# Performance work log

Hardware: AMD Instinct MI355X
Metric: run time of the kernel (lower is better)

## Reference

```python
import jax, jax.numpy as jnp
import numpy as np

DN = ('NCHW', 'OIHW', 'NCHW')

def _conv(x, w, groups=1, padding=0):
    return jax.lax.conv_general_dilated(
        x, w, window_strides=(1, 1), padding=[(padding, padding)] * 2,
        dimension_numbers=DN, feature_group_count=groups)

def _bn(x, scale, shift):
    # precomputed inference BN: x * scale + shift, per channel (NCHW)
    return x * scale[None, :, None, None] + shift[None, :, None, None]

def _channel_shuffle(x, g):
    n, c, h, w = x.shape
    return x.reshape(n, g, c // g, h, w).transpose(0, 2, 1, 3, 4).reshape(n, c, h, w)

def setup_inputs() -> dict:
    key = jax.random.key(0)
    ks = jax.random.split(key, 13)
    N, Cin, H, W = 32, 240, 56, 56
    Cout, G = 480, 3
    mid = Cout // 4  # 120
    inp = {
        'x': jax.random.normal(ks[0], (N, Cin, H, W), jnp.float32),
        'w1': jax.random.normal(ks[1], (mid, Cin // G, 1, 1), jnp.float32) * 0.05,
        'scale1': jax.random.uniform(ks[2], (mid,), jnp.float32, 0.5, 1.5),
        'shift1': jax.random.normal(ks[3], (mid,), jnp.float32) * 0.1,
        'w2': jax.random.normal(ks[4], (mid, 1, 3, 3), jnp.float32) * 0.05,
        'scale2': jax.random.uniform(ks[5], (mid,), jnp.float32, 0.5, 1.5),
        'shift2': jax.random.normal(ks[6], (mid,), jnp.float32) * 0.1,
        'w3': jax.random.normal(ks[7], (Cout, mid // G, 1, 1), jnp.float32) * 0.05,
        'scale3': jax.random.uniform(ks[8], (Cout,), jnp.float32, 0.5, 1.5),
        'shift3': jax.random.normal(ks[9], (Cout,), jnp.float32) * 0.1,
        'wsc': jax.random.normal(ks[10], (Cout, Cin, 1, 1), jnp.float32) * 0.05,
        'scale_sc': jax.random.uniform(ks[11], (Cout,), jnp.float32, 0.5, 1.5),
        'shift_sc': jax.random.normal(ks[12], (Cout,), jnp.float32) * 0.1,
        'groups': G,
    }
    return inp

def reference(x, w1, scale1, shift1, w2, scale2, shift2, w3, scale3, shift3,
              wsc, scale_sc, shift_sc, groups):
    g = int(groups)
    mid = w1.shape[0]
    # conv1 (grouped 1x1) -> fused BN + ReLU
    y = _conv(x, w1, groups=g)
    y = jax.nn.relu(_bn(y, scale1, shift1))
    # conv2 (depthwise 3x3) -> fused BN + channel shuffle
    y = _conv(y, w2, groups=mid, padding=1)
    y = _channel_shuffle(_bn(y, scale2, shift2), g)
    # conv3 (grouped 1x1)
    y = _conv(y, w3, groups=g)
    # shortcut: 1x1 conv (in_channels != out_channels)
    z = _conv(x, wsc)
    # fused final: relu(BN3(y)) + BN_sc(z)
    return jax.nn.relu(_bn(y, scale3, shift3)) + _bn(z, scale_sc, shift_sc)
```

## Files before the change

kernel.cpp:

```cpp
#include <hip/hip_runtime.h>

typedef short bf16x8 __attribute__((ext_vector_type(8)));
typedef float f32x4 __attribute__((ext_vector_type(4)));

namespace {
constexpr int kN = 32;
constexpr int kCin = 240;
constexpr int kHW = 3136;
constexpr int kMid = 120;
constexpr int kCout = 480;
constexpr size_t kXbtBytes = (size_t)kN * kHW * 240 * 2;
constexpr size_t kY2Off = kXbtBytes;
constexpr size_t kY2Bytes = (size_t)kN * kHW * 120 * 2;
constexpr size_t kY1Off = kY2Off + kY2Bytes;
}

__device__ __align__(16) unsigned short g_w1b[3 * 48 * 96];
__device__ __align__(16) unsigned short g_wscb[480 * 256];
__device__ __align__(16) unsigned short g_w3b[480 * 64];

static __device__ __forceinline__ unsigned short f2b(float f) {
  unsigned u = __float_as_uint(f);
  u = (u + 0x7fffu + ((u >> 16) & 1u)) >> 16;
  return (unsigned short)u;
}
static __device__ __forceinline__ float b2f(unsigned short s) {
  return __uint_as_float(((unsigned)s) << 16);
}
static __device__ __forceinline__ f32x4 mfma16(bf16x8 a, bf16x8 b, f32x4 c) {
  return __builtin_amdgcn_mfma_f32_16x16x32_bf16(a, b, c, 0, 0, 0);
}

__global__ __launch_bounds__(256) void prep_weights(
    const float* __restrict__ w1, const float* __restrict__ wsc,
    const float* __restrict__ w3) {
  const int idx = blockIdx.x * 256 + threadIdx.x;
  if (idx < 3 * 48 * 96) {
    const int g = idx / (48 * 96), r = idx % (48 * 96), j = r / 96, c = r % 96;
    g_w1b[idx] =
        (j < 40 && c < 80) ? f2b(w1[(g * 40 + j) * 80 + c]) : (unsigned short)0;
  } else if (idx < 3 * 48 * 96 + 480 * 256) {
    const int i = idx - 3 * 48 * 96;
    const int co = i >> 8, c = i & 255;
    g_wscb[i] = (c < 240) ? f2b(wsc[co * 240 + c]) : (unsigned short)0;
  } else if (idx < 3 * 48 * 96 + 480 * 256 + 480 * 64) {
    const int i = idx - (3 * 48 * 96 + 480 * 256);
    const int co = i >> 6, s = i & 63;
    g_w3b[i] = (s < 40) ? f2b(w3[co * 40 + s]) : (unsigned short)0;
  }
}

__global__ __launch_bounds__(256) void transpose_cast_x(
    const float* __restrict__ x, unsigned short* __restrict__ xbt) {
  const int pt = blockIdx.x % 13;
  const int ct = (blockIdx.x / 13) % 15;
  const int n = blockIdx.x / (13 * 15);
  const int p = pt * 256 + threadIdx.x;
  if (p >= kHW) return;
  const float* xp = x + ((size_t)n * kCin + ct * 16) * kHW + p;
  unsigned short v[16];
#pragma unroll
  for (int r = 0; r < 16; ++r) v[r] = f2b(xp[(size_t)r * kHW]);
  unsigned short* dst = xbt + (size_t)(n * kHW + p) * 240 + ct * 16;
  *reinterpret_cast<int4*>(dst) = *reinterpret_cast<const int4*>(v);
  *reinterpret_cast<int4*>(dst + 8) = *reinterpret_cast<const int4*>(v + 8);
}

__global__ __launch_bounds__(256) void conv1_gemm(
    const unsigned short* __restrict__ xbt, const float* __restrict__ scale1,
    const float* __restrict__ shift1, unsigned short* __restrict__ y1b) {
  const int pt = blockIdx.x % 49;
  const int g = (blockIdx.x / 49) % 3;
  const int n = blockIdx.x / (49 * 3);
  const int P0 = pt * 64;
  const int lane = threadIdx.x & 63;
  const int wv = threadIdx.x >> 6;
  const int l15 = lane & 15, quad = lane >> 4;

  f32x4 acc[3];
#pragma unroll
  for (int nt = 0; nt < 3; ++nt) acc[nt] = (f32x4){0.f, 0.f, 0.f, 0.f};

  const unsigned short* abase =
      xbt + (size_t)(n * kHW + P0 + wv * 16 + l15) * 240 + g * 80 + quad * 8;
  const unsigned short* bbase = g_w1b + (g * 48 + l15) * 96 + quad * 8;
#pragma unroll
  for (int ks = 0; ks < 3; ++ks) {
    const bf16x8 a = *reinterpret_cast<const bf16x8*>(abase + ks * 32);
#pragma unroll
    for (int nt = 0; nt < 3; ++nt) {
      const bf16x8 b =
          *reinterpret_cast<const bf16x8*>(bbase + nt * 16 * 96 + ks * 32);
      acc[nt] = mfma16(a, b, acc[nt]);
    }
  }

  __shared__ unsigned short lds[48 * 72];
#pragma unroll
  for (int nt = 0; nt < 3; ++nt) {
    const int j = nt * 16 + l15;
    if (j < 40) {
      const int c = g * 40 + j;
      const float sc = scale1[c], sh = shift1[c];
#pragma unroll
      for (int r = 0; r < 4; ++r) {
        float v = fmaf(acc[nt][r], sc, sh);
        v = v > 0.f ? v : 0.f;
        lds[j * 72 + wv * 16 + quad * 4 + r] = f2b(v);
      }
    }
  }
  __syncthreads();
  unsigned short* yb = y1b + ((size_t)n * kMid + g * 40) * kHW;
#pragma unroll
  for (int i = 0; i < 10; ++i) {
    const int e = threadIdx.x + i * 256;
    const int c = e >> 6, pp = e & 63;
    yb[(size_t)c * kHW + P0 + pp] = lds[c * 72 + pp];
  }
}

__global__ __launch_bounds__(256) void dw_bn_shuffle(
    const unsigned short* __restrict__ y1b, const float* __restrict__ w2,
    const float* __restrict__ scale2, const float* __restrict__ shift2,
    unsigned short* __restrict__ y2t) {
  const int h = blockIdx.x % 56;
  const int n = blockIdx.x / 56;
  __shared__ unsigned short lds[120 * 58];
  const unsigned short* yb = y1b + (size_t)n * kMid * kHW;
  for (int idx = threadIdx.x; idx < 120 * 56; idx += 256) {
    const int c = idx / 56, w = idx % 56;
    float acc = 0.f;
    const unsigned short* ip = yb + (size_t)c * kHW;
    const float* wp = w2 + c * 9;
#pragma unroll
    for (int dy = 0; dy < 3; ++dy) {
      const int hh = h + dy - 1;
      if (hh < 0 || hh >= 56) continue;
#pragma unroll
      for (int dx = 0; dx < 3; ++dx) {
        const int ww = w + dx - 1;
        if (ww < 0 || ww >= 56) continue;
        acc = fmaf(b2f(ip[hh * 56 + ww]), wp[dy * 3 + dx], acc);
      }
    }
    const float v = fmaf(acc, scale2[c], shift2[c]);
    const int cn = (c % 40) * 3 + c / 40;
    lds[cn * 58 + w] = f2b(v);
  }
  __syncthreads();
  unsigned short* dst = y2t + (size_t)(n * kHW + h * 56) * 120;
  for (int e = threadIdx.x; e < 56 * 120; e += 256)
    dst[e] = lds[(e % 120) * 58 + (e / 120)];
}

__global__ __launch_bounds__(256) void conv3_sc_gemm(
    const unsigned short* __restrict__ xbt,
    const unsigned short* __restrict__ y2t, const float* __restrict__ scale3,
    const float* __restrict__ shift3, const float* __restrict__ ssc,
    const float* __restrict__ bsc, float* __restrict__ out) {
  const int pt = blockIdx.x % 49;
  const int cb = (blockIdx.x / 49) % 3;
  const int n = blockIdx.x / (49 * 3);
  const int P0 = pt * 64;
  const int lane = threadIdx.x & 63;
  const int wv = threadIdx.x >> 6;
  const int mh = wv & 1, nh = wv >> 1;
  const int l15 = lane & 15, quad = lane >> 4;

  f32x4 acc_sc[2][5], acc_c3[2][5];
#pragma unroll
  for (int ms = 0; ms < 2; ++ms)
#pragma unroll
    for (int nt = 0; nt < 5; ++nt) {
      acc_sc[ms][nt] = (f32x4){0.f, 0.f, 0.f, 0.f};
      acc_c3[ms][nt] = (f32x4){0.f, 0.f, 0.f, 0.f};
    }

  const int co_row = cb * 160 + nh * 80 + l15;
  {
    const size_t prow = (size_t)(n * kHW + P0 + mh * 32 + l15) * 240;
    const unsigned short* a0 = xbt + prow + quad * 8;
    const unsigned short* a1 = xbt + prow + 16 * 240 + quad * 8;
    const unsigned short* b0 = g_wscb + co_row * 256 + quad * 8;
#pragma unroll
    for (int ks = 0; ks < 8; ++ks) {
      const bf16x8 A0 = *reinterpret_cast<const bf16x8*>(a0 + ks * 32);
      const bf16x8 A1 = *reinterpret_cast<const bf16x8*>(a1 + ks * 32);
#pragma unroll
      for (int nt = 0; nt < 5; ++nt) {
        const bf16x8 B =
            *reinterpret_cast<const bf16x8*>(b0 + nt * 16 * 256 + ks * 32);
        acc_sc[0][nt] = mfma16(A0, B, acc_sc[0][nt]);
        acc_sc[1][nt] = mfma16(A1, B, acc_sc[1][nt]);
      }
    }
  }
  {
    const size_t qrow = (size_t)(n * kHW + P0 + mh * 32 + l15) * 120 + cb * 40;
    const unsigned short* a0 = y2t + qrow + quad * 8;
    const unsigned short* a1 = y2t + qrow + 16 * 120 + quad * 8;
    const unsigned short* b3 = g_w3b + co_row * 64 + quad * 8;
#pragma unroll
    for (int ks = 0; ks < 2; ++ks) {
      const bf16x8 A0 = *reinterpret_cast<const bf16x8*>(a0 + ks * 32);
      const bf16x8 A1 = *reinterpret_cast<const bf16x8*>(a1 + ks * 32);
#pragma unroll
      for (int nt = 0; nt < 5; ++nt) {
        const bf16x8 B =
            *reinterpret_cast<const bf16x8*>(b3 + nt * 16 * 64 + ks * 32);
        acc_c3[0][nt] = mfma16(A0, B, acc_c3[0][nt]);
        acc_c3[1][nt] = mfma16(A1, B, acc_c3[1][nt]);
      }
    }
  }
  float* ob = out + (size_t)n * kCout * kHW;
#pragma unroll
  for (int nt = 0; nt < 5; ++nt) {
    const int co = cb * 160 + nh * 80 + nt * 16 + l15;
    const float s3 = scale3[co], h3 = shift3[co];
    const float s_ = ssc[co], h_ = bsc[co];
#pragma unroll
    for (int ms = 0; ms < 2; ++ms) {
      float4 r;
      float* op = ob + (size_t)co * kHW + P0 + mh * 32 + ms * 16 + quad * 4;
      float* rp = reinterpret_cast<float*>(&r);
#pragma unroll
      for (int r4 = 0; r4 < 4; ++r4) {
        float v3 = fmaf(acc_c3[ms][nt][r4], s3, h3);
        v3 = v3 > 0.f ? v3 : 0.f;
        rp[r4] = v3 + fmaf(acc_sc[ms][nt][r4], s_, h_);
      }
      *reinterpret_cast<float4*>(op) = r;
    }
  }
}

extern "C" void kernel_launch(void* const* d_in, const int* in_sizes, int n_in,
                              void* d_out, int out_size, void* d_ws,
                              size_t ws_size, hipStream_t stream) {
  const float* x = (const float*)d_in[0];
  const float* w1 = (const float*)d_in[1];
  const float* scale1 = (const float*)d_in[2];
  const float* shift1 = (const float*)d_in[3];
  const float* w2 = (const float*)d_in[4];
  const float* scale2 = (const float*)d_in[5];
  const float* shift2 = (const float*)d_in[6];
  const float* w3 = (const float*)d_in[7];
  const float* scale3 = (const float*)d_in[8];
  const float* shift3 = (const float*)d_in[9];
  const float* wsc = (const float*)d_in[10];
  const float* ssc = (const float*)d_in[11];
  const float* bsc = (const float*)d_in[12];
  float* out = (float*)d_out;

  unsigned short* xbt = (unsigned short*)d_ws;
  unsigned short* y2t = (unsigned short*)((char*)d_ws + kY2Off);
  unsigned short* y1b = (unsigned short*)((char*)d_ws + kY1Off);

  prep_weights<<<654, 256, 0, stream>>>(w1, wsc, w3);
  transpose_cast_x<<<32 * 15 * 13, 256, 0, stream>>>(x, xbt);
  conv1_gemm<<<32 * 3 * 49, 256, 0, stream>>>(xbt, scale1, shift1, y1b);
  dw_bn_shuffle<<<32 * 56, 256, 0, stream>>>(y1b, w2, scale2, shift2, y2t);
  conv3_sc_gemm<<<32 * 3 * 49, 256, 0, stream>>>(xbt, y2t, scale3, shift3, ssc,
                                                 bsc, out);
}
```

Baseline: 533.1 us.

## Fuse conv1 into depthwise kernel, tile-interleave activations, merge conv3/shortcut accumulators

Rewrites the pipeline. Activations are stored in an MFMA-friendly interleaved 16-pixel tile layout. The grouped 1x1 conv1 is fused into the depthwise 3x3 kernel, which recomputes conv1 for the needed rows into LDS instead of writing and re-reading a y1 buffer. The final GEMM folds the conv3 BN/ReLU result into a single accumulator by pre-dividing by the shortcut scale and uses larger pixel tiles across batch boundaries. This removes one intermediate round trip through global memory and halves accumulator registers, at the cost of redundant conv1 work on halo rows, larger LDS use, and a division by scale_sc that fails if that scale is zero.

Result: faster. 479.7 us (-10.0%).

```diff
diff --git a/kernel.cpp b/kernel.cpp
--- a/kernel.cpp
+++ b/kernel.cpp
@@ -4,135 +4,150 @@
 typedef float f32x4 __attribute__((ext_vector_type(4)));
 
 namespace {
-constexpr int kN = 32;
-constexpr int kCin = 240;
 constexpr int kHW = 3136;
-constexpr int kMid = 120;
-constexpr int kCout = 480;
-constexpr size_t kXbtBytes = (size_t)kN * kHW * 240 * 2;
-constexpr size_t kY2Off = kXbtBytes;
-constexpr size_t kY2Bytes = (size_t)kN * kHW * 120 * 2;
-constexpr size_t kY1Off = kY2Off + kY2Bytes;
-}
-
-__device__ __align__(16) unsigned short g_w1b[3 * 48 * 96];
-__device__ __align__(16) unsigned short g_wscb[480 * 256];
-__device__ __align__(16) unsigned short g_w3b[480 * 64];
+constexpr int kNPx = 32 * kHW;
+constexpr int kPtiles = kNPx / 16;
+constexpr size_t kXbiShorts = (size_t)kPtiles * 4096;
+}
+
+__device__ __align__(16) unsigned short g_w1i[3 * 4 * 48 * 32];
+__device__ __align__(16) unsigned short g_wsci[8 * 480 * 32];
+__device__ __align__(16) unsigned short g_w3i[2 * 480 * 32];
 
 static __device__ __forceinline__ unsigned short f2b(float f) {
   unsigned u = __float_as_uint(f);
   u = (u + 0x7fffu + ((u >> 16) & 1u)) >> 16;
   return (unsigned short)u;
 }
-static __device__ __forceinline__ float b2f(unsigned short s) {
-  return __uint_as_float(((unsigned)s) << 16);
-}
 static __device__ __forceinline__ f32x4 mfma16(bf16x8 a, bf16x8 b, f32x4 c) {
   return __builtin_amdgcn_mfma_f32_16x16x32_bf16(a, b, c, 0, 0, 0);
+}
+static __device__ __forceinline__ bf16x8 ldg8(const unsigned short* p) {
+  return *reinterpret_cast<const bf16x8*>(p);
 }
 
 __global__ __launch_bounds__(256) void prep_weights(
     const float* __restrict__ w1, const float* __restrict__ wsc,
     const float* __restrict__ w3) {
   const int idx = blockIdx.x * 256 + threadIdx.x;
-  if (idx < 3 * 48 * 96) {
-    const int g = idx / (48 * 96), r = idx % (48 * 96), j = r / 96, c = r % 96;
-    g_w1b[idx] =
-        (j < 40 && c < 80) ? f2b(w1[(g * 40 + j) * 80 + c]) : (unsigned short)0;
-  } else if (idx < 3 * 48 * 96 + 480 * 256) {
-    const int i = idx - 3 * 48 * 96;
-    const int co = i >> 8, c = i & 255;
-    g_wscb[i] = (c < 240) ? f2b(wsc[co * 240 + c]) : (unsigned short)0;
-  } else if (idx < 3 * 48 * 96 + 480 * 256 + 480 * 64) {
-    const int i = idx - (3 * 48 * 96 + 480 * 256);
-    const int co = i >> 6, s = i & 63;
-    g_w3b[i] = (s < 40) ? f2b(w3[co * 40 + s]) : (unsigned short)0;
-  }
-}
-
-__global__ __launch_bounds__(256) void transpose_cast_x(
-    const float* __restrict__ x, unsigned short* __restrict__ xbt) {
-  const int pt = blockIdx.x % 13;
-  const int ct = (blockIdx.x / 13) % 15;
-  const int n = blockIdx.x / (13 * 15);
-  const int p = pt * 256 + threadIdx.x;
-  if (p >= kHW) return;
-  const float* xp = x + ((size_t)n * kCin + ct * 16) * kHW + p;
-  unsigned short v[16];
-#pragma unroll
-  for (int r = 0; r < 16; ++r) v[r] = f2b(xp[(size_t)r * kHW]);
-  unsigned short* dst = xbt + (size_t)(n * kHW + p) * 240 + ct * 16;
-  *reinterpret_cast<int4*>(dst) = *reinterpret_cast<const int4*>(v);
-  *reinterpret_cast<int4*>(dst + 8) = *reinterpret_cast<const int4*>(v + 8);
-}
-
-__global__ __launch_bounds__(256) void conv1_gemm(
-    const unsigned short* __restrict__ xbt, const float* __restrict__ scale1,
-    const float* __restrict__ shift1, unsigned short* __restrict__ y1b) {
-  const int pt = blockIdx.x % 49;
-  const int g = (blockIdx.x / 49) % 3;
-  const int n = blockIdx.x / (49 * 3);
-  const int P0 = pt * 64;
+  if (idx < 18432) {
+    const int g = idx / 6144, r = idx % 6144, kb = r / 1536;
+    const int j = (r % 1536) / 32, k = r % 32;
+    const int gk = g * 64 + kb * 32 + k;
+    const int c = gk - g * 80;
+    unsigned short v = 0;
+    if (j < 40 && c >= 0 && c < 80) v = f2b(w1[(g * 40 + j) * 80 + c]);
+    g_w1i[idx] = v;
+  } else if (idx < 18432 + 122880) {
+    const int i = idx - 18432;
+    const int kb = i / 15360, co = (i % 15360) / 32, k = i % 32;
+    const int c = kb * 32 + k;
+    g_wsci[i] = (c < 240) ? f2b(wsc[co * 240 + c]) : (unsigned short)0;
+  } else if (idx < 18432 + 122880 + 30720) {
+    const int i = idx - 141312;
+    const int kb = i / 15360, co = (i % 15360) / 32, k = i % 32;
+    const int cb = co / 160;
+    const int s = cb * 32 + kb * 32 + k - cb * 40;
+    g_w3i[i] = (s >= 0 && s < 40) ? f2b(w3[co * 40 + s]) : (unsigned short)0;
+  }
+}
+
+__global__ __launch_bounds__(256) void transpose_interleave(
+    const float* __restrict__ x, unsigned short* __restrict__ xbi) {
+  const int P0 = blockIdx.x * 64;
+  const int px_loc = threadIdx.x >> 2, part = threadIdx.x & 3;
+  const int P = P0 + px_loc;
+  const int n = P / kHW, hw = P % kHW;
+  const int pt = px_loc >> 4, l = px_loc & 15;
+  unsigned short* dst =
+      xbi + ((size_t)(P0 / 16) + pt) * 4096 + l * 32 + part * 8;
+  const float* xp = x + ((size_t)n * 240) * kHW + hw;
+#pragma unroll
+  for (int kb = 0; kb < 8; ++kb) {
+    unsigned short v[8];
+#pragma unroll
+    for (int j = 0; j < 8; ++j) {
+      const int c = kb * 32 + part * 8 + j;
+      v[j] = (c < 240) ? f2b(xp[(size_t)c * kHW]) : (unsigned short)0;
+    }
+    *reinterpret_cast<uint4*>(dst + kb * 512) =
+        *reinterpret_cast<const uint4*>(v);
+  }
+}
+
+__global__ __launch_bounds__(256) void conv1_dw_fused(
+    const unsigned short* __restrict__ xbi, const float* __restrict__ scale1,
+    const float* __restrict__ shift1, const float* __restrict__ w2,
+    const float* __restrict__ scale2, const float* __restrict__ shift2,
+    unsigned short* __restrict__ y2i) {
+  const int h = blockIdx.x % 56;
+  const int n = blockIdx.x / 56;
+  const int A0 = (h > 0) ? (((h - 1) * 56) & ~15) : 0;
+
+  __shared__ unsigned short lds_y1[192 * 120];
+  __shared__ float lds_w2[9 * 120];
+  __shared__ float lds_s2[120], lds_h2[120];
+
+  for (int i = threadIdx.x; i < 9 * 120; i += 256) {
+    const int tap = i / 120, c = i % 120;
+    lds_w2[i] = w2[c * 9 + tap];
+  }
+  if (threadIdx.x < 120) {
+    lds_s2[threadIdx.x] = scale2[threadIdx.x];
+    lds_h2[threadIdx.x] = shift2[threadIdx.x];
+  }
+
   const int lane = threadIdx.x & 63;
   const int wv = threadIdx.x >> 6;
   const int l15 = lane & 15, quad = lane >> 4;
-
-  f32x4 acc[3];
-#pragma unroll
-  for (int nt = 0; nt < 3; ++nt) acc[nt] = (f32x4){0.f, 0.f, 0.f, 0.f};
-
-  const unsigned short* abase =
-      xbt + (size_t)(n * kHW + P0 + wv * 16 + l15) * 240 + g * 80 + quad * 8;
-  const unsigned short* bbase = g_w1b + (g * 48 + l15) * 96 + quad * 8;
-#pragma unroll
-  for (int ks = 0; ks < 3; ++ks) {
-    const bf16x8 a = *reinterpret_cast<const bf16x8*>(abase + ks * 32);
+  const size_t PT = (size_t)(n * kHW + A0) / 16 + wv * 3;
+
+#pragma unroll
+  for (int g = 0; g < 3; ++g) {
+    f32x4 acc[3][3];
+#pragma unroll
+    for (int mt = 0; mt < 3; ++mt)
+#pragma unroll
+      for (int nt = 0; nt < 3; ++nt) acc[mt][nt] = (f32x4){0.f, 0.f, 0.f, 0.f};
+#pragma unroll
+    for (int kb = 0; kb < 4; ++kb) {
+      const int kbi = 2 * g + kb;
+      bf16x8 A[3];
+#pragma unroll
+      for (int mt = 0; mt < 3; ++mt)
+        A[mt] = ldg8(xbi + (PT + mt) * 4096 + kbi * 512 + l15 * 32 + quad * 8);
+#pragma unroll
+      for (int nt = 0; nt < 3; ++nt) {
+        const bf16x8 B = ldg8(g_w1i + (((g * 4 + kb) * 48) + nt * 16 + l15) * 32 +
+                              quad * 8);
+#pragma unroll
+        for (int mt = 0; mt < 3; ++mt) acc[mt][nt] = mfma16(A[mt], B, acc[mt][nt]);
+      }
+    }
 #pragma unroll
     for (int nt = 0; nt < 3; ++nt) {
-      const bf16x8 b =
-          *reinterpret_cast<const bf16x8*>(bbase + nt * 16 * 96 + ks * 32);
-      acc[nt] = mfma16(a, b, acc[nt]);
-    }
-  }
-
-  __shared__ unsigned short lds[48 * 72];
-#pragma unroll
-  for (int nt = 0; nt < 3; ++nt) {
-    const int j = nt * 16 + l15;
-    if (j < 40) {
-      const int c = g * 40 + j;
-      const float sc = scale1[c], sh = shift1[c];
-#pragma unroll
-      for (int r = 0; r < 4; ++r) {
-        float v = fmaf(acc[nt][r], sc, sh);
-        v = v > 0.f ? v : 0.f;
-        lds[j * 72 + wv * 16 + quad * 4 + r] = f2b(v);
+      const int j = nt * 16 + l15;
+      if (j < 40) {
+        const int c = g * 40 + j;
+        const float sc = scale1[c], sh = shift1[c];
+#pragma unroll
+        for (int mt = 0; mt < 3; ++mt) {
+          const int pxb = wv * 48 + mt * 16 + quad * 4;
+#pragma unroll
+          for (int r = 0; r < 4; ++r) {
+            float v = fmaf(acc[mt][nt][r], sc, sh);
+            v = v > 0.f ? v : 0.f;
+            lds_y1[(pxb + r) * 120 + c] = f2b(v);
+          }
+        }
       }
     }
   }
   __syncthreads();
-  unsigned short* yb = y1b + ((size_t)n * kMid + g * 40) * kHW;
-#pragma unroll
-  for (int i = 0; i < 10; ++i) {
-    const int e = threadIdx.x + i * 256;
-    const int c = e >> 6, pp = e & 63;
-    yb[(size_t)c * kHW + P0 + pp] = lds[c * 72 + pp];
-  }
-}
-
-__global__ __launch_bounds__(256) void dw_bn_shuffle(
-    const unsigned short* __restrict__ y1b, const float* __restrict__ w2,
-    const float* __restrict__ scale2, const float* __restrict__ shift2,
-    unsigned short* __restrict__ y2t) {
-  const int h = blockIdx.x % 56;
-  const int n = blockIdx.x / 56;
-  __shared__ unsigned short lds[120 * 58];
-  const unsigned short* yb = y1b + (size_t)n * kMid * kHW;
-  for (int idx = threadIdx.x; idx < 120 * 56; idx += 256) {
-    const int c = idx / 56, w = idx % 56;
-    float acc = 0.f;
-    const unsigned short* ip = yb + (size_t)c * kHW;
-    const float* wp = w2 + c * 9;
+
+  for (int idx = threadIdx.x; idx < 56 * 120; idx += 256) {
+    const int c = idx % 120, w = idx / 120;
+    float a = 0.f;
 #pragma unroll
     for (int dy = 0; dy < 3; ++dy) {
       const int hh = h + dy - 1;
@@ -141,97 +156,100 @@
       for (int dx = 0; dx < 3; ++dx) {
         const int ww = w + dx - 1;
         if (ww < 0 || ww >= 56) continue;
-        acc = fmaf(b2f(ip[hh * 56 + ww]), wp[dy * 3 + dx], acc);
-      }
-    }
-    const float v = fmaf(acc, scale2[c], shift2[c]);
+        const int pl = hh * 56 + ww - A0;
+        a = fmaf(__uint_as_float((unsigned)lds_y1[pl * 120 + c] << 16),
+                 lds_w2[(dy * 3 + dx) * 120 + c], a);
+      }
+    }
+    const float v = fmaf(a, lds_s2[c], lds_h2[c]);
     const int cn = (c % 40) * 3 + c / 40;
-    lds[cn * 58 + w] = f2b(v);
-  }
-  __syncthreads();
-  unsigned short* dst = y2t + (size_t)(n * kHW + h * 56) * 120;
-  for (int e = threadIdx.x; e < 56 * 120; e += 256)
-    dst[e] = lds[(e % 120) * 58 + (e / 120)];
-}
-
-__global__ __launch_bounds__(256) void conv3_sc_gemm(
-    const unsigned short* __restrict__ xbt,
-    const unsigned short* __restrict__ y2t, const float* __restrict__ scale3,
+    const int P = n * kHW + h * 56 + w;
+    y2i[((size_t)(P >> 4)) * 2048 + (cn >> 5) * 512 + (P & 15) * 32 +
+        (cn & 31)] = f2b(v);
+  }
+}
+
+__global__ __launch_bounds__(256, 3) void conv3_sc_gemm(
+    const unsigned short* __restrict__ xbi,
+    const unsigned short* __restrict__ y2i, const float* __restrict__ scale3,
     const float* __restrict__ shift3, const float* __restrict__ ssc,
     const float* __restrict__ bsc, float* __restrict__ out) {
-  const int pt = blockIdx.x % 49;
-  const int cb = (blockIdx.x / 49) % 3;
-  const int n = blockIdx.x / (49 * 3);
-  const int P0 = pt * 64;
+  const int pxb = blockIdx.x % 784;
+  const int cb = blockIdx.x / 784;
+  const int P0 = pxb * 128;
   const int lane = threadIdx.x & 63;
   const int wv = threadIdx.x >> 6;
   const int mh = wv & 1, nh = wv >> 1;
   const int l15 = lane & 15, quad = lane >> 4;
-
-  f32x4 acc_sc[2][5], acc_c3[2][5];
-#pragma unroll
-  for (int ms = 0; ms < 2; ++ms)
+  const int cbase = cb * 160 + nh * 80;
+
+  f32x4 acc[4][5];
+#pragma unroll
+  for (int mt = 0; mt < 4; ++mt)
+#pragma unroll
+    for (int nt = 0; nt < 5; ++nt) acc[mt][nt] = (f32x4){0.f, 0.f, 0.f, 0.f};
+
+  const size_t PT = (size_t)(P0 / 16) + mh * 4;
+
+#pragma unroll
+  for (int kb = 0; kb < 2; ++kb) {
+    const int kbi = cb + kb;
+    bf16x8 A[4];
+#pragma unroll
+    for (int mt = 0; mt < 4; ++mt)
+      A[mt] = ldg8(y2i + (PT + mt) * 2048 + kbi * 512 + l15 * 32 + quad * 8);
 #pragma unroll
     for (int nt = 0; nt < 5; ++nt) {
-      acc_sc[ms][nt] = (f32x4){0.f, 0.f, 0.f, 0.f};
-      acc_c3[ms][nt] = (f32x4){0.f, 0.f, 0.f, 0.f};
-    }
-
-  const int co_row = cb * 160 + nh * 80 + l15;
-  {
-    const size_t prow = (size_t)(n * kHW + P0 + mh * 32 + l15) * 240;
-    const unsigned short* a0 = xbt + prow + quad * 8;
-    const unsigned short* a1 = xbt + prow + 16 * 240 + quad * 8;
-    const unsigned short* b0 = g_wscb + co_row * 256 + quad * 8;
-#pragma unroll
-    for (int ks = 0; ks < 8; ++ks) {
-      const bf16x8 A0 = *reinterpret_cast<const bf16x8*>(a0 + ks * 32);
-      const bf16x8 A1 = *reinterpret_cast<const bf16x8*>(a1 + ks * 32);
-#pragma unroll
-      for (int nt = 0; nt < 5; ++nt) {
-        const bf16x8 B =
-            *reinterpret_cast<const bf16x8*>(b0 + nt * 16 * 256 + ks * 32);
-        acc_sc[0][nt] = mfma16(A0, B, acc_sc[0][nt]);
-        acc_sc[1][nt] = mfma16(A1, B, acc_sc[1][nt]);
-      }
-    }
-  }
-  {
-    const size_t qrow = (size_t)(n * kHW + P0 + mh * 32 + l15) * 120 + cb * 40;
-    const unsigned short* a0 = y2t + qrow + quad * 8;
-    const unsigned short* a1 = y2t + qrow + 16 * 120 + quad * 8;
-    const unsigned short* b3 = g_w3b + co_row * 64 + quad * 8;
-#pragma unroll
-    for (int ks = 0; ks < 2; ++ks) {
-      const bf16x8 A0 = *reinterpret_cast<const bf16x8*>(a0 + ks * 32);
-      const bf16x8 A1 = *reinterpret_cast<const bf16x8*>(a1 + ks * 32);
-#pragma unroll
-      for (int nt = 0; nt < 5; ++nt) {
-        const bf16x8 B =
-            *reinterpret_cast<const bf16x8*>(b3 + nt * 16 * 64 + ks * 32);
-        acc_c3[0][nt] = mfma16(A0, B, acc_c3[0][nt]);
-        acc_c3[1][nt] = mfma16(A1, B, acc_c3[1][nt]);
-      }
-    }
-  }
-  float* ob = out + (size_t)n * kCout * kHW;
+      const bf16x8 B =
+          ldg8(g_w3i + ((kb * 480) + cbase + nt * 16 + l15) * 32 + quad * 8);
+#pragma unroll
+      for (int mt = 0; mt < 4; ++mt) acc[mt][nt] = mfma16(A[mt], B, acc[mt][nt]);
+    }
+  }
+
 #pragma unroll
   for (int nt = 0; nt < 5; ++nt) {
-    const int co = cb * 160 + nh * 80 + nt * 16 + l15;
+    const int co = cbase + nt * 16 + l15;
     const float s3 = scale3[co], h3 = shift3[co];
-    const float s_ = ssc[co], h_ = bsc[co];
-#pragma unroll
-    for (int ms = 0; ms < 2; ++ms) {
+    const float is = 1.0f / ssc[co], h_ = bsc[co];
+#pragma unroll
+    for (int mt = 0; mt < 4; ++mt)
+#pragma unroll
+      for (int r = 0; r < 4; ++r) {
+        float v3 = fmaf(acc[mt][nt][r], s3, h3);
+        v3 = v3 > 0.f ? v3 : 0.f;
+        acc[mt][nt][r] = (v3 + h_) * is;
+      }
+  }
+
+  for (int kb = 0; kb < 8; ++kb) {
+    bf16x8 A[4];
+#pragma unroll
+    for (int mt = 0; mt < 4; ++mt)
+      A[mt] = ldg8(xbi + (PT + mt) * 4096 + kb * 512 + l15 * 32 + quad * 8);
+#pragma unroll
+    for (int nt = 0; nt < 5; ++nt) {
+      const bf16x8 B =
+          ldg8(g_wsci + ((kb * 480) + cbase + nt * 16 + l15) * 32 + quad * 8);
+#pragma unroll
+      for (int mt = 0; mt < 4; ++mt) acc[mt][nt] = mfma16(A[mt], B, acc[mt][nt]);
+    }
+  }
+
+#pragma unroll
+  for (int mt = 0; mt < 4; ++mt) {
+    const int P = P0 + mh * 64 + mt * 16 + quad * 4;
+    const int n = P / kHW, hw = P % kHW;
+    float* ob = out + (size_t)n * 480 * kHW + hw;
+#pragma unroll
+    for (int nt = 0; nt < 5; ++nt) {
+      const int co = cbase + nt * 16 + l15;
+      const float s_ = ssc[co];
       float4 r;
-      float* op = ob + (size_t)co * kHW + P0 + mh * 32 + ms * 16 + quad * 4;
       float* rp = reinterpret_cast<float*>(&r);
 #pragma unroll
-      for (int r4 = 0; r4 < 4; ++r4) {
-        float v3 = fmaf(acc_c3[ms][nt][r4], s3, h3);
-        v3 = v3 > 0.f ? v3 : 0.f;
-        rp[r4] = v3 + fmaf(acc_sc[ms][nt][r4], s_, h_);
-      }
-      *reinterpret_cast<float4*>(op) = r;
+      for (int r4 = 0; r4 < 4; ++r4) rp[r4] = s_ * acc[mt][nt][r4];
+      *reinterpret_cast<float4*>(ob + (size_t)co * kHW) = r;
     }
   }
 }
@@ -254,14 +272,13 @@
   const float* bsc = (const float*)d_in[12];
   float* out = (float*)d_out;
 
-  unsigned short* xbt = (unsigned short*)d_ws;
-  unsigned short* y2t = (unsigned short*)((char*)d_ws + kY2Off);
-  unsigned short* y1b = (unsigned short*)((char*)d_ws + kY1Off);
-
-  prep_weights<<<654, 256, 0, stream>>>(w1, wsc, w3);
-  transpose_cast_x<<<32 * 15 * 13, 256, 0, stream>>>(x, xbt);
-  conv1_gemm<<<32 * 3 * 49, 256, 0, stream>>>(xbt, scale1, shift1, y1b);
-  dw_bn_shuffle<<<32 * 56, 256, 0, stream>>>(y1b, w2, scale2, shift2, y2t);
-  conv3_sc_gemm<<<32 * 3 * 49, 256, 0, stream>>>(xbt, y2t, scale3, shift3, ssc,
-                                                 bsc, out);
-}
+  unsigned short* xbi = (unsigned short*)d_ws;
+  unsigned short* y2i = xbi + kXbiShorts;
+
+  prep_weights<<<672, 256, 0, stream>>>(w1, wsc, w3);
+  transpose_interleave<<<kNPx / 64, 256, 0, stream>>>(x, xbi);
+  conv1_dw_fused<<<32 * 56, 256, 0, stream>>>(xbi, scale1, shift1, w2, scale2,
+                                              shift2, y2i);
+  conv3_sc_gemm<<<784 * 3, 256, 0, stream>>>(xbi, y2i, scale3, shift3, ssc,
+                                             bsc, out);
+}
```
